# Performance work log

Hardware: AMD Instinct MI355X
Metric: run time of the kernel (lower is better)

## Reference

```python
import jax, jax.numpy as jnp
import numpy as np

DIM = 3072
NUM_HEADS = 24
HEAD_DIM = 128
SEQ = 2048
BATCH = 1
EPS = 1e-6


def _make_rope(seq_len: int, head_dim: int):
    # Standard RoPE angles; cos/sin laid out per interleaved-pair convention
    # (each frequency repeated for the (real, imag) pair), shape [S, head_dim].
    half = head_dim // 2
    inv_freq = 1.0 / (10000.0 ** (np.arange(0, half, dtype=np.float32) / half))
    t = np.arange(seq_len, dtype=np.float32)
    freqs = np.outer(t, inv_freq)  # [S, half]
    freqs = np.repeat(freqs, 2, axis=-1)  # [S, head_dim], pairs share the angle
    return jnp.asarray(np.cos(freqs)), jnp.asarray(np.sin(freqs))


def setup_inputs() -> dict:
    key = jax.random.key(0)
    ks = jax.random.split(key, 8)
    inner = NUM_HEADS * HEAD_DIM
    s = 0.02
    hidden_states = jax.random.normal(ks[0], (BATCH, SEQ, DIM), dtype=jnp.float32)
    wq = jax.random.normal(ks[1], (inner, DIM), dtype=jnp.float32) * s
    wk = jax.random.normal(ks[2], (inner, DIM), dtype=jnp.float32) * s
    wv = jax.random.normal(ks[3], (inner, DIM), dtype=jnp.float32) * s
    bq = jax.random.normal(ks[4], (inner,), dtype=jnp.float32) * s
    bk = jax.random.normal(ks[5], (inner,), dtype=jnp.float32) * s
    bv = jax.random.normal(ks[6], (inner,), dtype=jnp.float32) * s
    norm_q_w = jnp.ones((HEAD_DIM,), dtype=jnp.float32)
    norm_k_w = jnp.ones((HEAD_DIM,), dtype=jnp.float32)
    cos, sin = _make_rope(SEQ, HEAD_DIM)
    return {
        "hidden_states": hidden_states,
        "wq": wq, "bq": bq, "wk": wk, "bk": bk, "wv": wv, "bv": bv,
        "norm_q_w": norm_q_w, "norm_k_w": norm_k_w,
        "cos": cos, "sin": sin,
    }


def _rms_norm(x, w, eps=EPS):
    # RMSNorm over the last (head_dim) axis.
    var = jnp.mean(jnp.square(x), axis=-1, keepdims=True)
    return x * jax.lax.rsqrt(var + eps) * w


def _apply_rope(x, cos, sin):
    # x: [B, S, H, D]; cos/sin: [S, D]. Interleaved-pair rotation
    # (diffusers apply_rotary_emb, use_real_unbind_dim=-1).
    xr = x[..., 0::2]
    xi = x[..., 1::2]
    rot = jnp.stack([-xi, xr], axis=-1).reshape(x.shape)
    c = cos[None, :, None, :]
    s = sin[None, :, None, :]
    return x * c + rot * s


def reference(hidden_states, wq, bq, wk, bk, wv, bv, norm_q_w, norm_k_w, cos, sin):
    B, S, _ = hidden_states.shape
    H, D = NUM_HEADS, HEAD_DIM
    # QKV projections (ColumnParallelLinear with tp_size=1)
    q = (hidden_states @ wq.T + bq).reshape(B, S, H, D)
    k = (hidden_states @ wk.T + bk).reshape(B, S, H, D)
    v = (hidden_states @ wv.T + bv).reshape(B, S, H, D)
    # qk-norm then RoPE
    q = _apply_rope(_rms_norm(q, norm_q_w), cos, sin)
    k = _apply_rope(_rms_norm(k, norm_k_w), cos, sin)
    # Non-causal full attention
    scale = 1.0 / jnp.sqrt(jnp.asarray(D, dtype=q.dtype))
    scores = jnp.einsum("bqhd,bkhd->bhqk", q, k) * scale
    probs = jax.nn.softmax(scores, axis=-1)
    out = jnp.einsum("bhqk,bkhd->bqhd", probs, v)
    return out.reshape(B, S, H * D).astype(q.dtype)
```

## Files before the change

### kernel.cpp

```cpp
#include <hip/hip_runtime.h>

#define S_LEN 2048
#define DIMSZ 3072
#define NHEAD 24
#define HDIM 128
#define NQKV 9216
#define QSCALE 0.08838834764831845f
#define FMAX 12.0f

typedef unsigned short u16;
typedef unsigned int u32;
typedef __attribute__((ext_vector_type(8))) short short8;
typedef __attribute__((ext_vector_type(4))) float f32x4;

__device__ __forceinline__ u16 f2bf(float f) {
    u32 u = __float_as_uint(f);
    u32 r = (u + 0x7fffu + ((u >> 16) & 1u)) >> 16;
    return (u16)r;
}
__device__ __forceinline__ float bf2f(u16 u) {
    return __uint_as_float((u32)u << 16);
}

__device__ __forceinline__ void lds16(u16* lds, const u16* g) {
    __builtin_amdgcn_global_load_lds((const __attribute__((address_space(1))) u32*)g,
                                     (__attribute__((address_space(3))) u32*)lds, 16, 0, 0);
}

__global__ void k_f2bf4(const float4* __restrict__ src, u16* __restrict__ dst, int n4) {
    int i = blockIdx.x * blockDim.x + threadIdx.x;
    if (i >= n4) return;
    float4 v = src[i];
    u32 lo = (u32)f2bf(v.x) | ((u32)f2bf(v.y) << 16);
    u32 hi = (u32)f2bf(v.z) | ((u32)f2bf(v.w) << 16);
    uint2 p; p.x = lo; p.y = hi;
    *(uint2*)(dst + (size_t)i * 4) = p;
}

__global__ __launch_bounds__(256, 2) void k_gemm(const u16* __restrict__ A, const u16* __restrict__ W,
                                                 u16* __restrict__ C) {
    __shared__ __align__(16) u16 As[2][128 * 32];
    __shared__ __align__(16) u16 Bs[2][192 * 32];
    const int tid = threadIdx.x, wave = tid >> 6, lane = tid & 63;
    const int bm = blockIdx.x / 48, bn = blockIdx.x % 48;
    const int wm = wave >> 1, wn = wave & 1;
    const int frow = lane & 15, fk = lane >> 4;
    const u16* baseA = A + (size_t)(bm * 128) * DIMSZ;
    const u16* baseW = W + (size_t)(bn * 192) * DIMSZ;

    auto stage = [&](int b, int kt) {
#pragma unroll
        for (int j = 0; j < 2; ++j) {
            int flat = j * 256 + tid, row = flat >> 2, ch = flat & 3;
            lds16(&As[b][flat * 8], baseA + (size_t)row * DIMSZ + kt * 32 + ((ch ^ ((row >> 1) & 3)) * 8));
        }
#pragma unroll
        for (int j = 0; j < 3; ++j) {
            int flat = j * 256 + tid, row = flat >> 2, ch = flat & 3;
            lds16(&Bs[b][flat * 8], baseW + (size_t)row * DIMSZ + kt * 32 + ((ch ^ ((row >> 1) & 3)) * 8));
        }
    };

    stage(0, 0); stage(1, 1);
    asm volatile("s_waitcnt vmcnt(5)");
    __builtin_amdgcn_s_barrier();

    f32x4 acc[4][6] = {};
    for (int T = 0; T < 96; ++T) {
        const int b = T & 1;
        const u16* LA = As[b];
        const u16* LB = Bs[b];
        short8 af[4], bf[6];
#pragma unroll
        for (int mf = 0; mf < 4; ++mf) {
            int row = wm * 64 + mf * 16 + frow;
            af[mf] = *(const short8*)&LA[row * 32 + ((fk ^ ((row >> 1) & 3)) * 8)];
        }
#pragma unroll
        for (int nf = 0; nf < 6; ++nf) {
            int row = wn * 96 + nf * 16 + frow;
            bf[nf] = *(const short8*)&LB[row * 32 + ((fk ^ ((row >> 1) & 3)) * 8)];
        }
        __builtin_amdgcn_s_barrier();
        __builtin_amdgcn_s_setprio(1);
#pragma unroll
        for (int mf = 0; mf < 4; ++mf)
#pragma unroll
            for (int nf = 0; nf < 6; ++nf)
                acc[mf][nf] = __builtin_amdgcn_mfma_f32_16x16x32_bf16(af[mf], bf[nf], acc[mf][nf], 0, 0, 0);
        __builtin_amdgcn_s_setprio(0);
        __builtin_amdgcn_s_barrier();
        if (T < 94) {
            stage(b, T + 2);
            asm volatile("s_waitcnt vmcnt(5)");
            __builtin_amdgcn_s_barrier();
        } else if (T == 94) {
            asm volatile("s_waitcnt vmcnt(0)");
            __builtin_amdgcn_s_barrier();
        }
    }

#pragma unroll
    for (int mf = 0; mf < 4; ++mf) {
#pragma unroll
        for (int nf = 0; nf < 6; ++nf) {
            int n = bn * 192 + wn * 96 + nf * 16 + frow;
#pragma unroll
            for (int i = 0; i < 4; ++i) {
                int m = bm * 128 + wm * 64 + mf * 16 + fk * 4 + i;
                C[(size_t)m * NQKV + n] = f2bf(acc[mf][nf][i]);
            }
        }
    }
}

__global__ void k_post(const u16* __restrict__ qkv, const float* __restrict__ nw_q,
                       const float* __restrict__ nw_k, const float* __restrict__ bq,
                       const float* __restrict__ bk, const float* __restrict__ bv,
                       const float* __restrict__ cosT, const float* __restrict__ sinT,
                       u16* __restrict__ Qb, u16* __restrict__ Kb, u16* __restrict__ Vt) {
    const int wave = threadIdx.x >> 6, lane = threadIdx.x & 63;
    const int s = blockIdx.x * 4 + wave;
    const int h = blockIdx.y;
    const int d0 = 2 * lane, d1 = 2 * lane + 1;
    const float c = cosT[s * HDIM + d0], sn = sinT[s * HDIM + d0];
    const u16* r0 = qkv + (size_t)s * NQKV + h * HDIM;
    {
        float x0 = bf2f(r0[d0]) + bq[h * HDIM + d0];
        float x1 = bf2f(r0[d1]) + bq[h * HDIM + d1];
        float ss = x0 * x0 + x1 * x1;
        for (int m = 1; m < 64; m <<= 1) ss += __shfl_xor(ss, m);
        float r = rsqrtf(ss * (1.0f / 128.0f) + 1e-6f);
        x0 *= r * nw_q[d0]; x1 *= r * nw_q[d1];
        float o0 = (x0 * c - x1 * sn) * QSCALE;
        float o1 = (x1 * c + x0 * sn) * QSCALE;
        u32 p = (u32)f2bf(o0) | ((u32)f2bf(o1) << 16);
        *(u32*)&Qb[((size_t)h * S_LEN + s) * HDIM + d0] = p;
    }
    {
        float x0 = bf2f(r0[3072 + d0]) + bk[h * HDIM + d0];
        float x1 = bf2f(r0[3072 + d1]) + bk[h * HDIM + d1];
        float ss = x0 * x0 + x1 * x1;
        for (int m = 1; m < 64; m <<= 1) ss += __shfl_xor(ss, m);
        float r = rsqrtf(ss * (1.0f / 128.0f) + 1e-6f);
        x0 *= r * nw_k[d0]; x1 *= r * nw_k[d1];
        float o0 = x0 * c - x1 * sn;
        float o1 = x1 * c + x0 * sn;
        u32 p = (u32)f2bf(o0) | ((u32)f2bf(o1) << 16);
        *(u32*)&Kb[((size_t)h * S_LEN + s) * HDIM + d0] = p;
    }
    {
        float v0 = bf2f(r0[6144 + d0]) + bv[h * HDIM + d0];
        float v1 = bf2f(r0[6144 + d1]) + bv[h * HDIM + d1];
        Vt[((size_t)h * HDIM + d0) * S_LEN + s] = f2bf(v0);
        Vt[((size_t)h * HDIM + d1) * S_LEN + s] = f2bf(v1);
    }
}

__global__ __launch_bounds__(256, 2) void k_attn(const u16* __restrict__ Qb, const u16* __restrict__ Kb,
                                                 const u16* __restrict__ Vt, float* __restrict__ oP,
                                                 float* __restrict__ lP) {
    __shared__ __align__(16) u16 Ks[2][64 * 128];
    __shared__ __align__(16) u16 Vs[2][128 * 64];
    __shared__ __align__(16) u16 Ps[4][32 * 64];
    const int wave = threadIdx.x >> 6, lane = threadIdx.x & 63;
    const int half = blockIdx.x & 1, unit = blockIdx.x >> 1;
    const int h = unit >> 4, qb = unit & 15;
    const int kt0 = half * 16;
    const int frow = lane & 15, fk = lane >> 4;

    short8 qf[2][4];
#pragma unroll
    for (int qg = 0; qg < 2; ++qg) {
        const u16* qbase = Qb + ((size_t)h * S_LEN + qb * 128 + wave * 32 + qg * 16 + frow) * HDIM + fk * 8;
#pragma unroll
        for (int ks = 0; ks < 4; ++ks) qf[qg][ks] = *(const short8*)(qbase + ks * 32);
    }

    f32x4 o[2][8] = {};
    float l_p[2][4] = {};

#define STAGE(buf, kt)                                                                       \
    {                                                                                        \
        _Pragma("unroll") for (int c = 0; c < 4; ++c) {                                      \
            int fi = (wave * 4 + c) * 64 + lane;                                             \
            {                                                                                \
                int r = fi >> 4, ch = fi & 15;                                               \
                lds16(Ks[buf] + (wave * 4 + c) * 512,                                        \
                      Kb + ((size_t)h * S_LEN + (kt) * 64 + r) * HDIM + ((ch ^ (r & 15)) * 8)); \
            }                                                                                \
            {                                                                                \
                int r = fi >> 3, ch = fi & 7;                                                \
                lds16(Vs[buf] + (wave * 4 + c) * 512,                                        \
                      Vt + ((size_t)h * HDIM + r) * S_LEN + (kt) * 64 + ((ch ^ (r & 7)) * 8)); \
            }                                                                                \
        }                                                                                    \
    }

    STAGE(0, kt0);
    __syncthreads();
    int cur = 0;

    for (int kt = kt0; kt < kt0 + 16; ++kt) {
        if (kt + 1 < kt0 + 16) STAGE(cur ^ 1, kt + 1);
        f32x4 sacc[2][4] = {};
#pragma unroll
        for (int nf = 0; nf < 4; ++nf) {
#pragma unroll
            for (int ks = 0; ks < 4; ++ks) {
                short8 kf = *(const short8*)&Ks[cur][(nf * 16 + frow) * 128 + (((ks * 4 + fk) ^ frow) & 15) * 8];
#pragma unroll
                for (int qg = 0; qg < 2; ++qg)
                    sacc[qg][nf] = __builtin_amdgcn_mfma_f32_16x16x32_bf16(qf[qg][ks], kf, sacc[qg][nf], 0, 0, 0);
            }
        }
#pragma unroll
        for (int qg = 0; qg < 2; ++qg)
#pragma unroll
            for (int nf = 0; nf < 4; ++nf)
#pragma unroll
                for (int i = 0; i < 4; ++i) {
                    float p = __expf(sacc[qg][nf][i] - FMAX);
                    l_p[qg][i] += p;
                    int row = qg * 16 + fk * 4 + i, col = nf * 16 + frow;
                    Ps[wave][row * 64 + (((col >> 3) ^ (row & 7)) << 3) + (col & 7)] = f2bf(p);
                }
#pragma unroll
        for (int ks = 0; ks < 2; ++ks) {
            short8 pf[2];
#pragma unroll
            for (int qg = 0; qg < 2; ++qg)
                pf[qg] = *(const short8*)&Ps[wave][(qg * 16 + frow) * 64 + (((ks * 4 + fk) ^ (frow & 7)) & 7) * 8];
#pragma unroll
            for (int nf8 = 0; nf8 < 8; ++nf8) {
                short8 vf = *(const short8*)&Vs[cur][(nf8 * 16 + frow) * 64 + (((ks * 4 + fk) ^ (frow & 7)) & 7) * 8];
#pragma unroll
                for (int qg = 0; qg < 2; ++qg)
                    o[qg][nf8] = __builtin_amdgcn_mfma_f32_16x16x32_bf16(pf[qg], vf, o[qg][nf8], 0, 0, 0);
            }
        }
        __syncthreads();
        cur ^= 1;
    }
#undef STAGE

#pragma unroll
    for (int msk = 1; msk < 16; msk <<= 1)
#pragma unroll
        for (int qg = 0; qg < 2; ++qg)
#pragma unroll
            for (int i = 0; i < 4; ++i) l_p[qg][i] += __shfl_xor(l_p[qg][i], msk);

    float* oH = oP + (size_t)half * S_LEN * DIMSZ;
#pragma unroll
    for (int qg = 0; qg < 2; ++qg)
#pragma unroll
        for (int nf8 = 0; nf8 < 8; ++nf8)
#pragma unroll
            for (int i = 0; i < 4; ++i) {
                int srow = qb * 128 + wave * 32 + qg * 16 + fk * 4 + i;
                oH[(size_t)srow * DIMSZ + h * HDIM + nf8 * 16 + frow] = o[qg][nf8][i];
            }
    if (frow == 0) {
#pragma unroll
        for (int qg = 0; qg < 2; ++qg)
#pragma unroll
            for (int i = 0; i < 4; ++i) {
                int srow = qb * 128 + wave * 32 + qg * 16 + fk * 4 + i;
                lP[(size_t)half * NHEAD * S_LEN + h * S_LEN + srow] = l_p[qg][i];
            }
    }
}

__global__ void k_fin(const float* __restrict__ oP, const float* __restrict__ lP,
                      float* __restrict__ out) {
    int idx = blockIdx.x * 256 + threadIdx.x;
    int s = idx / DIMSZ, hd = idx - s * DIMSZ, h = hd >> 7;
    float l = lP[h * S_LEN + s] + lP[NHEAD * S_LEN + h * S_LEN + s];
    out[idx] = (oP[idx] + oP[(size_t)S_LEN * DIMSZ + idx]) / l;
}

extern "C" void kernel_launch(void* const* d_in, const int* in_sizes, int n_in,
                              void* d_out, int out_size, void* d_ws, size_t ws_size,
                              hipStream_t stream) {
    const float* hs = (const float*)d_in[0];
    const float* wq = (const float*)d_in[1];
    const float* bq = (const float*)d_in[2];
    const float* wk = (const float*)d_in[3];
    const float* bk = (const float*)d_in[4];
    const float* wv = (const float*)d_in[5];
    const float* bv = (const float*)d_in[6];
    const float* nq = (const float*)d_in[7];
    const float* nk = (const float*)d_in[8];
    const float* cosT = (const float*)d_in[9];
    const float* sinT = (const float*)d_in[10];
    float* out = (float*)d_out;

    char* ws = (char*)d_ws;
    u16* hs_b = (u16*)(ws);
    u16* w_b = (u16*)(ws + 12582912);
    u16* qkv = (u16*)(ws + 69206016);
    u16* Qb = (u16*)(ws + 106954752);
    u16* Kb = (u16*)(ws + 119537664);
    u16* Vt = (u16*)(ws + 132120576);
    float* oP = (float*)(ws + 144703488);
    float* lP = (float*)(ws + 195035136);

    k_f2bf4<<<6144, 256, 0, stream>>>((const float4*)hs, hs_b, 1572864);
    k_f2bf4<<<9216, 256, 0, stream>>>((const float4*)wq, w_b, 2359296);
    k_f2bf4<<<9216, 256, 0, stream>>>((const float4*)wk, w_b + 9437184, 2359296);
    k_f2bf4<<<9216, 256, 0, stream>>>((const float4*)wv, w_b + 18874368, 2359296);

    k_gemm<<<dim3(768), 256, 0, stream>>>(hs_b, w_b, qkv);

    k_post<<<dim3(512, 24), 256, 0, stream>>>(qkv, nq, nk, bq, bk, bv, cosT, sinT, Qb, Kb, Vt);

    k_attn<<<dim3(768), 256, 0, stream>>>(Qb, Kb, Vt, oP, lP);
    k_fin<<<dim3(24576), 256, 0, stream>>>(oP, lP, out);
}
```

Measured before the change: 328.4 us.

## Prefetch GEMM fragments across iterations and drop attention KV split with finalize kernel

The GEMM main loop is unrolled by two with ping-pong register fragments, so LDS reads for the next tile are issued before the MFMAs on the current tile, with the barrier and stage ordering rearranged to match. The attention kernel stops splitting the key range into two halves: each workgroup processes all 32 key tiles, normalizes by the row sum itself and writes the final output. Blocks are remapped so that eight consecutive blocks go to different heads. This removes the partial-output round trip through memory and the separate k_fin launch, but halves the attention grid to 384 workgroups, which may leave compute units underused.

Result: slower. 344.6 us (+4.9%).

```diff
diff --git a/kernel.cpp b/kernel.cpp
--- a/kernel.cpp
+++ b/kernel.cpp
@@ -61,44 +61,51 @@
         }
     };
 
+#define FRAG_READ(af_, bf_, LA_, LB_)                                                    \
+    _Pragma("unroll") for (int mf = 0; mf < 4; ++mf) {                                   \
+        int row = wm * 64 + mf * 16 + frow;                                              \
+        af_[mf] = *(const short8*)&LA_[row * 32 + ((fk ^ ((row >> 1) & 3)) * 8)];        \
+    }                                                                                    \
+    _Pragma("unroll") for (int nf = 0; nf < 6; ++nf) {                                   \
+        int row = wn * 96 + nf * 16 + frow;                                              \
+        bf_[nf] = *(const short8*)&LB_[row * 32 + ((fk ^ ((row >> 1) & 3)) * 8)];        \
+    }
+
     stage(0, 0); stage(1, 1);
     asm volatile("s_waitcnt vmcnt(5)");
     __builtin_amdgcn_s_barrier();
 
     f32x4 acc[4][6] = {};
-    for (int T = 0; T < 96; ++T) {
-        const int b = T & 1;
-        const u16* LA = As[b];
-        const u16* LB = Bs[b];
-        short8 af[4], bf[6];
-#pragma unroll
-        for (int mf = 0; mf < 4; ++mf) {
-            int row = wm * 64 + mf * 16 + frow;
-            af[mf] = *(const short8*)&LA[row * 32 + ((fk ^ ((row >> 1) & 3)) * 8)];
-        }
-#pragma unroll
-        for (int nf = 0; nf < 6; ++nf) {
-            int row = wn * 96 + nf * 16 + frow;
-            bf[nf] = *(const short8*)&LB[row * 32 + ((fk ^ ((row >> 1) & 3)) * 8)];
-        }
-        __builtin_amdgcn_s_barrier();
-        __builtin_amdgcn_s_setprio(1);
-#pragma unroll
-        for (int mf = 0; mf < 4; ++mf)
-#pragma unroll
-            for (int nf = 0; nf < 6; ++nf)
-                acc[mf][nf] = __builtin_amdgcn_mfma_f32_16x16x32_bf16(af[mf], bf[nf], acc[mf][nf], 0, 0, 0);
-        __builtin_amdgcn_s_setprio(0);
-        __builtin_amdgcn_s_barrier();
-        if (T < 94) {
-            stage(b, T + 2);
-            asm volatile("s_waitcnt vmcnt(5)");
-            __builtin_amdgcn_s_barrier();
-        } else if (T == 94) {
-            asm volatile("s_waitcnt vmcnt(0)");
-            __builtin_amdgcn_s_barrier();
-        }
-    }
+    short8 afA[4], bfA[6], afB[4], bfB[6];
+    FRAG_READ(afA, bfA, As[0], Bs[0])
+
+#define GBODY(T, afC, bfC, afN, bfN)                                                     \
+    {                                                                                    \
+        const int b_ = (T) & 1;                                                          \
+        asm volatile("s_waitcnt lgkmcnt(0)");        \
+        __builtin_amdgcn_s_barrier();                \
+        if ((T) < 94) {                                                                  \
+            stage(b_, (T) + 2);                               \
+            asm volatile("s_waitcnt vmcnt(5)");           \
+        } else if ((T) == 94) {                                                          \
+            asm volatile("s_waitcnt vmcnt(0)");                                          \
+        }                                                                                \
+        __builtin_amdgcn_s_barrier();                     \
+        if ((T) < 95) { FRAG_READ(afN, bfN, As[b_ ^ 1], Bs[b_ ^ 1]) }                    \
+        __builtin_amdgcn_s_setprio(1);                                                   \
+        _Pragma("unroll") for (int mf = 0; mf < 4; ++mf)                                 \
+            _Pragma("unroll") for (int nf = 0; nf < 6; ++nf)                             \
+                acc[mf][nf] = __builtin_amdgcn_mfma_f32_16x16x32_bf16(                   \
+                    afC[mf], bfC[nf], acc[mf][nf], 0, 0, 0);                             \
+        __builtin_amdgcn_s_setprio(0);                                                   \
+    }
+
+    for (int T = 0; T < 96; T += 2) {
+        GBODY(T, afA, bfA, afB, bfB)
+        GBODY(T + 1, afB, bfB, afA, bfA)
+    }
+#undef GBODY
+#undef FRAG_READ
 
 #pragma unroll
     for (int mf = 0; mf < 4; ++mf) {
@@ -158,15 +165,13 @@
 }
 
 __global__ __launch_bounds__(256, 2) void k_attn(const u16* __restrict__ Qb, const u16* __restrict__ Kb,
-                                                 const u16* __restrict__ Vt, float* __restrict__ oP,
-                                                 float* __restrict__ lP) {
+                                                 const u16* __restrict__ Vt, float* __restrict__ out) {
     __shared__ __align__(16) u16 Ks[2][64 * 128];
     __shared__ __align__(16) u16 Vs[2][128 * 64];
     __shared__ __align__(16) u16 Ps[4][32 * 64];
     const int wave = threadIdx.x >> 6, lane = threadIdx.x & 63;
-    const int half = blockIdx.x & 1, unit = blockIdx.x >> 1;
-    const int h = unit >> 4, qb = unit & 15;
-    const int kt0 = half * 16;
+    const int wg = (blockIdx.x & 7) * 48 + (blockIdx.x >> 3);
+    const int h = wg >> 4, qb = wg & 15;
     const int frow = lane & 15, fk = lane >> 4;
 
     short8 qf[2][4];
@@ -197,12 +202,12 @@
         }                                                                                    \
     }
 
-    STAGE(0, kt0);
+    STAGE(0, 0);
     __syncthreads();
     int cur = 0;
 
-    for (int kt = kt0; kt < kt0 + 16; ++kt) {
-        if (kt + 1 < kt0 + 16) STAGE(cur ^ 1, kt + 1);
+    for (int kt = 0; kt < S_LEN / 64; ++kt) {
+        if (kt + 1 < S_LEN / 64) STAGE(cur ^ 1, kt + 1);
         f32x4 sacc[2][4] = {};
 #pragma unroll
         for (int nf = 0; nf < 4; ++nf) {
@@ -251,7 +256,6 @@
 #pragma unroll
             for (int i = 0; i < 4; ++i) l_p[qg][i] += __shfl_xor(l_p[qg][i], msk);
 
-    float* oH = oP + (size_t)half * S_LEN * DIMSZ;
 #pragma unroll
     for (int qg = 0; qg < 2; ++qg)
 #pragma unroll
@@ -259,25 +263,8 @@
 #pragma unroll
             for (int i = 0; i < 4; ++i) {
                 int srow = qb * 128 + wave * 32 + qg * 16 + fk * 4 + i;
-                oH[(size_t)srow * DIMSZ + h * HDIM + nf8 * 16 + frow] = o[qg][nf8][i];
+                out[(size_t)srow * DIMSZ + h * HDIM + nf8 * 16 + frow] = o[qg][nf8][i] / l_p[qg][i];
             }
-    if (frow == 0) {
-#pragma unroll
-        for (int qg = 0; qg < 2; ++qg)
-#pragma unroll
-            for (int i = 0; i < 4; ++i) {
-                int srow = qb * 128 + wave * 32 + qg * 16 + fk * 4 + i;
-                lP[(size_t)half * NHEAD * S_LEN + h * S_LEN + srow] = l_p[qg][i];
-            }
-    }
-}
-
-__global__ void k_fin(const float* __restrict__ oP, const float* __restrict__ lP,
-                      float* __restrict__ out) {
-    int idx = blockIdx.x * 256 + threadIdx.x;
-    int s = idx / DIMSZ, hd = idx - s * DIMSZ, h = hd >> 7;
-    float l = lP[h * S_LEN + s] + lP[NHEAD * S_LEN + h * S_LEN + s];
-    out[idx] = (oP[idx] + oP[(size_t)S_LEN * DIMSZ + idx]) / l;
 }
 
 extern "C" void kernel_launch(void* const* d_in, const int* in_sizes, int n_in,
@@ -303,8 +290,6 @@
     u16* Qb = (u16*)(ws + 106954752);
     u16* Kb = (u16*)(ws + 119537664);
     u16* Vt = (u16*)(ws + 132120576);
-    float* oP = (float*)(ws + 144703488);
-    float* lP = (float*)(ws + 195035136);
 
     k_f2bf4<<<6144, 256, 0, stream>>>((const float4*)hs, hs_b, 1572864);
     k_f2bf4<<<9216, 256, 0, stream>>>((const float4*)wq, w_b, 2359296);
@@ -315,6 +300,5 @@
 
     k_post<<<dim3(512, 24), 256, 0, stream>>>(qkv, nq, nk, bq, bk, bv, cosT, sinT, Qb, Kb, Vt);
 
-    k_attn<<<dim3(768), 256, 0, stream>>>(Qb, Kb, Vt, oP, lP);
-    k_fin<<<dim3(24576), 256, 0, stream>>>(oP, lP, out);
-}
+    k_attn<<<dim3(384), 256, 0, stream>>>(Qb, Kb, Vt, out);
+}
```
